# Performance work log

Measured on AMD Instinct MI355X. Metric: run time of the kernel, lower is better.

Reference implementation:

```python
import jax, jax.numpy as jnp
import numpy as np

V, E, U, D, B, T = 32000, 256, 512, 512, 32, 64


def setup_inputs() -> dict:
    key = jax.random.key(0)
    ks = jax.random.split(key, 12)
    g = lambda k, shape: (jax.random.normal(k, shape, jnp.float32) * 0.05)
    return dict(
        x=jax.random.randint(ks[0], (B, T), 0, V),
        emb=g(ks[1], (V, E)),
        Wxf=g(ks[2], (E, 4 * U)), Whf=g(ks[3], (U, 4 * U)), bf=jnp.zeros((4 * U,), jnp.float32),
        Wxb=g(ks[4], (E, 4 * U)), Whb=g(ks[5], (U, 4 * U)), bb=jnp.zeros((4 * U,), jnp.float32),
        W1=g(ks[6], (2 * U + D, 10)), b1=jnp.zeros((10,), jnp.float32),
        W2=g(ks[7], (10, 1)), b2=jnp.zeros((1,), jnp.float32),
        Wxd=g(ks[8], (2 * U, 4 * D)), Whd=g(ks[9], (D, 4 * D)), bd=jnp.zeros((4 * D,), jnp.float32),
        Wo=g(ks[10], (D, V)), bo=jnp.zeros((V,), jnp.float32),
    )


def lstm_cell(x_t, h, c, Wx, Wh, b):
    # Keras gate order: i, f, g(cell), o
    z = x_t @ Wx + h @ Wh + b
    i, f, g, o = jnp.split(z, 4, axis=-1)
    c = jax.nn.sigmoid(f) * c + jax.nn.sigmoid(i) * jnp.tanh(g)
    h = jax.nn.sigmoid(o) * jnp.tanh(c)
    return h, c


def lstm_seq(xs, Wx, Wh, b):
    # xs: [T, B, F] -> hidden states [T, B, units]
    units = Wh.shape[0]
    h0 = jnp.zeros((xs.shape[1], units), xs.dtype)

    def step(carry, x_t):
        h, c = lstm_cell(x_t, carry[0], carry[1], Wx, Wh, b)
        return (h, c), h

    _, hs = jax.lax.scan(step, (h0, h0), xs)
    return hs


def reference(x, emb, Wxf, Whf, bf, Wxb, Whb, bb, W1, b1, W2, b2, Wxd, Whd, bd, Wo, bo):
    Bsz, Tlen = x.shape
    xe = emb[x]                              # [B, T, E]
    xs = jnp.swapaxes(xe, 0, 1)              # [T, B, E]
    hf = lstm_seq(xs, Wxf, Whf, bf)          # forward direction
    hb = lstm_seq(xs[::-1], Wxb, Whb, bb)[::-1]  # backward direction
    a = jnp.swapaxes(jnp.concatenate([hf, hb], axis=-1), 0, 1)  # [B, T, 2U]
    du = Whd.shape[0]

    def dec_step(carry, _):
        h, c = carry
        s_rep = jnp.broadcast_to(h[:, None, :], (Bsz, Tlen, du))
        cat = jnp.concatenate([a, s_rep], axis=-1)              # [B, T, 2U+D]
        e = jax.nn.relu(jnp.tanh(cat @ W1 + b1) @ W2 + b2)      # [B, T, 1]
        score = jax.nn.softmax(e, axis=1)
        ctx = jnp.sum(score * a, axis=1)                        # [B, 2U]
        h, c = lstm_cell(ctx, h, c, Wxd, Whd, bd)
        out = jax.nn.softmax(h @ Wo + bo, axis=-1)              # [B, V]
        return (h, c), out

    init = (jnp.zeros((Bsz, du), a.dtype), jnp.zeros((Bsz, du), a.dtype))
    _, outs = jax.lax.scan(dec_step, init, None, length=Tlen)
    return jnp.swapaxes(outs, 0, 1)  # [B, T, V]
```

## Files before the change

### kernel.cpp

```cpp
#include <hip/hip_runtime.h>
#include <hip/hip_bf16.h>
#include <cstdint>

typedef float f32x4 __attribute__((ext_vector_type(4)));
typedef __bf16 bf16x8 __attribute__((ext_vector_type(8)));

__device__ __forceinline__ uint32_t bf1(float x) {
  uint32_t u = __float_as_uint(x);
  return (u + 0x7fffu + ((u >> 16) & 1u)) >> 16;
}
__device__ __forceinline__ uint32_t bpack(float lo, float hi) {
  return bf1(lo) | (bf1(hi) << 16);
}
__device__ __forceinline__ float blo(uint32_t u) { return __uint_as_float(u << 16); }
__device__ __forceinline__ float bhi(uint32_t u) { return __uint_as_float(u & 0xffff0000u); }
__device__ __forceinline__ float sigm(float x) {
  return __fdividef(1.f, 1.f + exp2f(x * -1.4426950408889634f));
}
__device__ __forceinline__ float tanhf_fast(float x) {
  float e2 = exp2f(x * 2.8853900817779268f);
  return 1.f - __fdividef(2.f, e2 + 1.f);
}

__device__ __forceinline__ float dot2bf(uint32_t a, uint32_t b, float acc) {
  asm("v_dot2_f32_bf16 %0, %1, %2, %0" : "+v"(acc) : "v"(a), "v"(b));
  return acc;
}

#define GLOAD_LDS16(g, l)                                                     \
  __builtin_amdgcn_global_load_lds(                                           \
      (const __attribute__((address_space(1))) void*)(g),                     \
      (__attribute__((address_space(3))) void*)(l), 16, 0, 0)

__global__ __launch_bounds__(256) void k0_pack(
    const float* __restrict__ Whf, const float* __restrict__ Whb,
    uint32_t* __restrict__ Wencp, const float* __restrict__ Whd,
    uint32_t* __restrict__ Wdp, const float* __restrict__ W1,
    uint32_t* __restrict__ W1pbAll)
{
  int bid = blockIdx.x;
  if (bid < 4096) {
    int p = bid * 256 + threadIdx.x;
    int j2 = p & 3, slot = (p >> 2) & 63, c = (p >> 8) & 15;
    int cg = (p >> 12) & 127, dir = p >> 19;
    int k = slot * 8 + j2 * 2;
    const float* W = dir ? Whb : Whf;
    int colg = (c >> 2) * 512 + cg * 4 + (c & 3);
    Wencp[p ^ ((c & 7) << 2)] =
        bpack(W[(size_t)k * 2048 + colg], W[(size_t)(k + 1) * 2048 + colg]);
  } else if (bid < 6144) {
    int p = (bid - 4096) * 256 + threadIdx.x;
    int e = p & 3, cc = (p >> 2) & 31, q4 = (p >> 7) & 63, ug = p >> 13;
    int k2 = 4 * q4 + e;
    int col = (cc >> 3) * 512 + ug * 8 + (cc & 7);
    int k = 2 * k2;
    Wdp[p] = bpack(Whd[(size_t)k * 2048 + col], Whd[(size_t)(k + 1) * 2048 + col]);
  } else {
    int p = (bid - 6144) * 256 + threadIdx.x;
    if (p < 9216) {
      int q = p / 12, j = p % 12;
      float v0 = (j < 10) ? W1[(size_t)(2 * q) * 10 + j] : 0.f;
      float v1 = (j < 10) ? W1[(size_t)(2 * q + 1) * 10 + j] : 0.f;
      W1pbAll[p] = bpack(v0, v1);
    }
  }
}

__global__ __launch_bounds__(256) void k1_embed_gemm(
    const int* __restrict__ x, const float* __restrict__ emb,
    const float* __restrict__ Wxf, const float* __restrict__ Wxb,
    const float* __restrict__ bfv, const float* __restrict__ bbv,
    float* __restrict__ Xf, float* __restrict__ Xb)
{
  __shared__ float As[32 * 260];
  __shared__ float Bs[32 * 128];
  __shared__ int xid[32];
  const int t = threadIdx.x;
  const int ty = blockIdx.y;
  const int c0 = blockIdx.x * 128;
  if (t < 32) xid[t] = x[t * 64 + ty];
  __syncthreads();
  for (int i = 0; i < 8; ++i) {
    int f4 = t + 256 * i;
    int r = f4 >> 6, k4 = (f4 & 63) << 2;
    float4 v = *(const float4*)(emb + (size_t)xid[r] * 256 + k4);
    *(float4*)(&As[r * 260 + k4]) = v;
  }
  const int isB = (c0 >= 2048);
  const float* Wsrc = isB ? Wxb : Wxf;
  const float* bias = isB ? bbv : bfv;
  const int cbase = c0 & 2047;
  float acc[4][4] = {};
  const int rq = t >> 5;
  const int cq = t & 31;
  for (int kc = 0; kc < 8; ++kc) {
    int k0 = kc * 32;
    __syncthreads();
    for (int i = 0; i < 4; ++i) {
      int f4 = t + 256 * i;
      int k = f4 >> 5, c4 = (f4 & 31) << 2;
      *(float4*)(&Bs[k * 128 + c4]) =
          *(const float4*)(Wsrc + (size_t)(k0 + k) * 2048 + cbase + c4);
    }
    __syncthreads();
#pragma unroll
    for (int kk = 0; kk < 32; ++kk) {
      float a0 = As[(4 * rq + 0) * 260 + k0 + kk];
      float a1 = As[(4 * rq + 1) * 260 + k0 + kk];
      float a2 = As[(4 * rq + 2) * 260 + k0 + kk];
      float a3 = As[(4 * rq + 3) * 260 + k0 + kk];
      float4 b = *(const float4*)(&Bs[kk * 128 + 4 * cq]);
      acc[0][0] += a0 * b.x; acc[0][1] += a0 * b.y; acc[0][2] += a0 * b.z; acc[0][3] += a0 * b.w;
      acc[1][0] += a1 * b.x; acc[1][1] += a1 * b.y; acc[1][2] += a1 * b.z; acc[1][3] += a1 * b.w;
      acc[2][0] += a2 * b.x; acc[2][1] += a2 * b.y; acc[2][2] += a2 * b.z; acc[2][3] += a2 * b.w;
      acc[3][0] += a3 * b.x; acc[3][1] += a3 * b.y; acc[3][2] += a3 * b.z; acc[3][3] += a3 * b.w;
    }
  }
  float* Xout = isB ? Xb : Xf;
  for (int i = 0; i < 4; ++i) {
    int c = cbase + 4 * cq + i;
    float bi = bias[c];
    for (int j = 0; j < 4; ++j) {
      int b_ = 4 * rq + j;
      Xout[((size_t)ty * 2048 + c) * 32 + b_] = acc[j][i] + bi;
    }
  }
}

__global__ __launch_bounds__(256) void k2_enc_step(
    const float* __restrict__ Xf, const float* __restrict__ Xb,
    const uint32_t* __restrict__ Wencp,
    const uint32_t* __restrict__ hfi, uint32_t* __restrict__ hfo,
    const uint32_t* __restrict__ hbi, uint32_t* __restrict__ hbo,
    float* __restrict__ cf, float* __restrict__ cb,
    ushort* __restrict__ aB, int step)
{
  __shared__ ushort Hs[16 * 512];
  __shared__ ushort Ws[16 * 512];
  __shared__ float zp[4 * 256];
  __shared__ float zx[256];
  __shared__ float zbuf[256];
  __shared__ float hl[64];
  const int t = threadIdx.x;
  const int dir = blockIdx.x >> 8;
  const int rh = (blockIdx.x >> 7) & 1;
  const int cg = blockIdx.x & 127;
  const int r0 = rh * 16, u0 = cg * 4;
  const float* XF = dir ? Xb : Xf;
  const uint32_t* hin = dir ? hbi : hfi;
  uint32_t* hout = dir ? hbo : hfo;
  float* cst = dir ? cb : cf;
  const int ta = dir ? (63 - step) : step;

  {
    const uint32_t* hinu = hin + r0 * 256;
    for (int i = 0; i < 4; ++i) {
      int b4 = (t >> 6) * 64 + 256 * i;
      GLOAD_LDS16(hinu + (size_t)(t + 256 * i) * 4, (uint32_t*)Hs + b4 * 4);
    }
    const uint32_t* wsrc = Wencp + ((size_t)dir * 128 + cg) * 4096;
    for (int i = 0; i < 4; ++i) {
      int b4 = (t >> 6) * 64 + 256 * i;
      GLOAD_LDS16(wsrc + (size_t)(t + 256 * i) * 4, (uint32_t*)Ws + b4 * 4);
    }
  }
  {
    int cl = t & 15, rl = t >> 4;
    int colg = (cl >> 2) * 512 + u0 + (cl & 3);
    zx[t] = XF[((size_t)ta * 2048 + colg) * 32 + r0 + rl];
  }
  __syncthreads();
  const int lane = t & 63, w = t >> 6;
  const int quad = lane >> 4, l15 = lane & 15;
  f32x4 acc = {};
#pragma unroll
  for (int mm = 0; mm < 4; ++mm) {
    int m = w * 4 + mm;
    int slot = m * 4 + quad;
    bf16x8 a = *(const bf16x8*)(Hs + l15 * 512 + (slot ^ (l15 & 7)) * 8);
    bf16x8 b = *(const bf16x8*)(Ws + l15 * 512 + (slot ^ (l15 & 7)) * 8);
    acc = __builtin_amdgcn_mfma_f32_16x16x32_bf16(a, b, acc, 0, 0, 0);
  }
#pragma unroll
  for (int reg = 0; reg < 4; ++reg)
    zp[w * 256 + (quad * 4 + reg) * 16 + l15] = acc[reg];
  __syncthreads();
  zbuf[t] = zp[t] + zp[256 + t] + zp[512 + t] + zp[768 + t] + zx[t];
  __syncthreads();
  if (t < 64) {
    int rl = t & 15, ui = t >> 4;
    int u = u0 + ui, r = r0 + rl;
    float zi = zbuf[rl * 16 + ui];
    float zf = zbuf[rl * 16 + 4 + ui];
    float zg = zbuf[rl * 16 + 8 + ui];
    float zo = zbuf[rl * 16 + 12 + ui];
    float cold = cst[u * 32 + r];
    float cn = sigm(zf) * cold + sigm(zi) * tanhf_fast(zg);
    float h = sigm(zo) * tanhf_fast(cn);
    cst[u * 32 + r] = cn;
    aB[((size_t)r * 64 + ta) * 1024 + dir * 512 + u] = (ushort)bf1(h);
    hl[rl * 4 + ui] = h;
  }
  __syncthreads();
  if (t < 16) {
    int r = r0 + t;
    uint32_t lo = bpack(hl[t * 4 + 0], hl[t * 4 + 1]);
    uint32_t hi = bpack(hl[t * 4 + 2], hl[t * 4 + 3]);
    uint32_t* dst = hout + r * 256 + (((cg >> 1) ^ (r & 7)) * 4) + (cg & 1) * 2;
    *(uint2*)dst = make_uint2(lo, hi);
  }
}

__global__ __launch_bounds__(256) void k5_aw1(
    const ushort* __restrict__ aB, const uint32_t* __restrict__ W1pbAll,
    const float* __restrict__ b1, float* __restrict__ aw1)
{
  __shared__ uint32_t ar[512];
  __shared__ float ps[16 * 17];
  const int t = threadIdx.x;
  const uint32_t* aBu = (const uint32_t*)aB;
  for (int m = blockIdx.x; m < 2048; m += gridDim.x) {
    __syncthreads();
    *(uint2*)(&ar[t * 2]) = *(const uint2*)(aBu + (size_t)m * 512 + t * 2);
    __syncthreads();
    int j = t & 15, part = t >> 4;
    int jj = j < 10 ? j : 0;
    float s = 0.f;
#pragma unroll 8
    for (int q = part * 32; q < part * 32 + 32; ++q)
      s = dot2bf(ar[q], W1pbAll[q * 12 + jj], s);
    ps[part * 17 + j] = s;
    __syncthreads();
    if (t < 16) {
      float sum = 0.f;
      if (t < 10) {
        for (int p = 0; p < 16; ++p) sum += ps[p * 17 + t];
        sum += b1[t];
      }
      aw1[m * 16 + t] = sum;
    }
  }
}

__global__ __launch_bounds__(256) void k_wxdT(
    const float* __restrict__ Wxd, ushort* __restrict__ WxdT)
{
  __shared__ float tile[64 * 65];
  const int t = threadIdx.x;
  const int n0 = blockIdx.x * 64, k0 = blockIdx.y * 64;
  for (int i = 0; i < 16; ++i) {
    int p = t + 256 * i;
    int kk = p >> 6, nn = p & 63;
    tile[kk * 65 + nn] = Wxd[(size_t)(k0 + kk) * 2048 + n0 + nn];
  }
  __syncthreads();
  for (int i = 0; i < 4; ++i) {
    int p = t + 256 * i;
    int nn = p >> 4, k4 = (p & 15) * 4;
    ushort4 o;
    o.x = (ushort)bf1(tile[(k4 + 0) * 65 + nn]);
    o.y = (ushort)bf1(tile[(k4 + 1) * 65 + nn]);
    o.z = (ushort)bf1(tile[(k4 + 2) * 65 + nn]);
    o.w = (ushort)bf1(tile[(k4 + 3) * 65 + nn]);
    *(ushort4*)(WxdT + (size_t)(n0 + nn) * 1024 + k0 + k4) = o;
  }
}

__global__ __launch_bounds__(256) void kA_aprime(
    const ushort* __restrict__ WxdT, const ushort* __restrict__ aB,
    uint32_t* __restrict__ ApTb)
{
  __shared__ ushort As[128 * 64];
  __shared__ ushort Bs[128 * 64];
  const int t = threadIdx.x;
  const int lane = t & 63, w = t >> 6;
  const int wr = w >> 1, wc = w & 1;
  const int m0 = blockIdx.y * 128, n0 = blockIdx.x * 128;
  const int lrow = lane >> 3, s = lane & 7;
  const int quad = lane >> 4, l15 = lane & 15;
  f32x4 acc[4][4] = {};
  for (int kc = 0; kc < 16; ++kc) {
    const int k0 = kc * 64;
    __syncthreads();
    for (int i = 0; i < 4; ++i) {
      int row = w * 32 + i * 8 + lrow;
      int k8 = s ^ (row & 7);
      GLOAD_LDS16(WxdT + (size_t)(m0 + row) * 1024 + k0 + k8 * 8,
                  As + (w * 32 + i * 8) * 64);
      GLOAD_LDS16(aB + (size_t)(n0 + row) * 1024 + k0 + k8 * 8,
                  Bs + (w * 32 + i * 8) * 64);
    }
    __syncthreads();
#pragma unroll
    for (int ks = 0; ks < 2; ++ks) {
      bf16x8 af[4], bfr[4];
      int kq = ks * 4 + quad;
#pragma unroll
      for (int mi = 0; mi < 4; ++mi) {
        int row = wr * 64 + mi * 16 + l15;
        int slot = kq ^ (row & 7);
        af[mi] = *(const bf16x8*)(As + row * 64 + slot * 8);
      }
#pragma unroll
      for (int ni = 0; ni < 4; ++ni) {
        int row = wc * 64 + ni * 16 + l15;
        int slot = kq ^ (row & 7);
        bfr[ni] = *(const bf16x8*)(Bs + row * 64 + slot * 8);
      }
#pragma unroll
      for (int mi = 0; mi < 4; ++mi)
#pragma unroll
        for (int ni = 0; ni < 4; ++ni)
          acc[mi][ni] = __builtin_amdgcn_mfma_f32_16x16x32_bf16(
              af[mi], bfr[ni], acc[mi][ni], 0, 0, 0);
    }
  }
#pragma unroll
  for (int mi = 0; mi < 4; ++mi) {
    int mbase = m0 + wr * 64 + mi * 16 + quad * 4;
#pragma unroll
    for (int reg = 0; reg < 4; ++reg) {
      int m = mbase + reg;
#pragma unroll
      for (int ni = 0; ni < 4; ++ni) {
        int n = n0 + wc * 64 + ni * 16 + l15;
        float v = acc[mi][ni][reg];
        float v2 = __shfl_xor(v, 1);
        if (!(l15 & 1))
          ApTb[(size_t)m * 1024 + (n >> 1)] = bpack(v, v2);
      }
    }
  }
}

__global__ __launch_bounds__(256) void k4_dec_step(
    const uint32_t* __restrict__ ApTb, const float* __restrict__ aw1,
    const uint32_t* __restrict__ W1pb, const float* __restrict__ W2,
    const float* __restrict__ b2, const uint32_t* __restrict__ hdp_in,
    const uint32_t* __restrict__ Wdp, const float* __restrict__ bd,
    uint32_t* __restrict__ hdp_out, float* __restrict__ cd,
    ushort* __restrict__ HsB, int step)
{
  __shared__ uint32_t W1s[256 * 12];
  __shared__ uint32_t hdT[1024];
  __shared__ uint32_t Wsp[8192];
  __shared__ float ph[64 * 4 * 12];
  __shared__ float hw1[4 * 12];
  __shared__ float esc[4 * 65];
  __shared__ uint32_t escp[4 * 33];
  __shared__ float pm[4 * 9];
  __shared__ float mrow[4], srow[4];
  __shared__ float w2s[12];
  __shared__ float zp[2][128];
  __shared__ float zbuf[4 * 33];
  __shared__ float hl[32];
  const int t = threadIdx.x;
  const int ug = blockIdx.x >> 3;
  const int rg = blockIdx.x & 7;
  const int u0 = ug * 8, r0 = rg * 4;
  for (int i = 0; i < 3; ++i) {
    int b4 = (t >> 6) * 64 + 256 * i;
    GLOAD_LDS16(W1pb + (size_t)(t + 256 * i) * 4, W1s + (size_t)b4 * 4);
  }
  {
    int q4 = t >> 2, rl0 = t & 3;
    int b4 = (t >> 6) * 64;
    GLOAD_LDS16(hdp_in + (size_t)(q4 * 32 + r0 + rl0) * 4, hdT + (size_t)b4 * 4);
  }
  if (t < 12) w2s[t] = (t < 10) ? W2[t] : 0.f;
  __syncthreads();
  {
    const uint32_t* wsrc = Wdp + (size_t)ug * 8192;
    for (int i = 0; i < 8; ++i) {
      int b4 = (t >> 6) * 64 + 256 * i;
      GLOAD_LDS16(wsrc + (size_t)(t + 256 * i) * 4, Wsp + (size_t)b4 * 4);
    }
  }
  {
    const int rl = t & 3, kp = t >> 2;
    const uint4* hd4 = (const uint4*)hdT;
    float acc[10] = {};
    {
      uint4 u4 = hd4[kp * 4 + rl];
      const uint32_t* w0 = &W1s[(4 * kp) * 12];
      const uint32_t* w1 = &W1s[(4 * kp + 1) * 12];
      const uint32_t* w2p = &W1s[(4 * kp + 2) * 12];
      const uint32_t* w3 = &W1s[(4 * kp + 3) * 12];
#pragma unroll
      for (int j = 0; j < 10; ++j) {
        acc[j] = dot2bf(u4.x, w0[j], acc[j]);
        acc[j] = dot2bf(u4.y, w1[j], acc[j]);
        acc[j] = dot2bf(u4.z, w2p[j], acc[j]);
        acc[j] = dot2bf(u4.w, w3[j], acc[j]);
      }
    }
#pragma unroll
    for (int j = 0; j < 10; ++j) ph[(kp * 4 + rl) * 12 + j] = acc[j];
  }
  __syncthreads();
  if (t < 40) {
    int rl = t / 10, j = t % 10;
    float s = 0.f;
#pragma unroll
    for (int p = 0; p < 64; ++p) s += ph[(p * 4 + rl) * 12 + j];
    hw1[rl * 12 + j] = s;
  }
  __syncthreads();
  const float b2v = b2[0];
  {
    int rl = t >> 6, tt = t & 63;
    size_t m = (size_t)(r0 + rl) * 64 + tt;
    const float4* aw = (const float4*)(aw1 + m * 16);
    float4 q0 = aw[0], q1 = aw[1], q2 = aw[2];
    const float* hw = &hw1[rl * 12];
    float e = b2v;
    e += tanhf_fast(q0.x + hw[0]) * w2s[0];
    e += tanhf_fast(q0.y + hw[1]) * w2s[1];
    e += tanhf_fast(q0.z + hw[2]) * w2s[2];
    e += tanhf_fast(q0.w + hw[3]) * w2s[3];
    e += tanhf_fast(q1.x + hw[4]) * w2s[4];
    e += tanhf_fast(q1.y + hw[5]) * w2s[5];
    e += tanhf_fast(q1.z + hw[6]) * w2s[6];
    e += tanhf_fast(q1.w + hw[7]) * w2s[7];
    e += tanhf_fast(q2.x + hw[8]) * w2s[8];
    e += tanhf_fast(q2.y + hw[9]) * w2s[9];
    esc[rl * 65 + tt] = fmaxf(e, 0.f);
  }
  __syncthreads();
  if (t < 32) {
    int rl = t >> 3, part = t & 7;
    float m = -1e30f;
    for (int i = 0; i < 8; ++i) m = fmaxf(m, esc[rl * 65 + part * 8 + i]);
    pm[rl * 9 + part] = m;
  }
  __syncthreads();
  if (t < 4) {
    float m = pm[t * 9];
    for (int p = 1; p < 8; ++p) m = fmaxf(m, pm[t * 9 + p]);
    mrow[t] = m;
  }
  __syncthreads();
  if (t < 32) {
    int rl = t >> 3, part = t & 7;
    float m = mrow[rl];
    float s = 0.f;
    for (int i = 0; i < 8; ++i) s += __expf(esc[rl * 65 + part * 8 + i] - m);
    pm[rl * 9 + part] = s;
  }
  __syncthreads();
  if (t < 4) {
    float s = 0.f;
    for (int p = 0; p < 8; ++p) s += pm[t * 9 + p];
    srow[t] = __fdividef(1.f, s);
  }
  __syncthreads();
  if (t < 128) {
    int rl = t >> 5, q = t & 31;
    float m = mrow[rl], s = srow[rl];
    float v0 = __expf(esc[rl * 65 + 2 * q] - m) * s;
    float v1 = __expf(esc[rl * 65 + 2 * q + 1] - m) * s;
    escp[rl * 33 + q] = bpack(v0, v1);
  }
  __syncthreads();
  {
    const int out = t & 127;
    const int ccB = out >> 2, rl = out & 3;
    const int kh = t >> 7;
    const int colg = (ccB >> 3) * 512 + u0 + (ccB & 7);
    float acc = 0.f;
    {
      const uint4* hd4 = (const uint4*)hdT;
      const uint4* wd4 = (const uint4*)Wsp;
#pragma unroll 8
      for (int q4 = kh * 32; q4 < kh * 32 + 32; ++q4) {
        uint4 ua = hd4[q4 * 4 + rl];
        uint4 ub = wd4[q4 * 32 + ccB];
        acc = dot2bf(ua.x, ub.x, acc);
        acc = dot2bf(ua.y, ub.y, acc);
        acc = dot2bf(ua.z, ub.z, acc);
        acc = dot2bf(ua.w, ub.w, acc);
      }
    }
    {
      const uint32_t* ap = ApTb + (size_t)colg * 1024 + (r0 + rl) * 32;
      const uint32_t* ep = &escp[rl * 33];
#pragma unroll
      for (int i8 = kh * 4; i8 < kh * 4 + 4; ++i8) {
        uint4 v = *(const uint4*)(ap + i8 * 4);
        acc = dot2bf(v.x, ep[4 * i8 + 0], acc);
        acc = dot2bf(v.y, ep[4 * i8 + 1], acc);
        acc = dot2bf(v.z, ep[4 * i8 + 2], acc);
        acc = dot2bf(v.w, ep[4 * i8 + 3], acc);
      }
    }
    zp[kh][out] = acc;
  }
  __syncthreads();
  if (t < 128) {
    int ccB = t >> 2, rl = t & 3;
    int colg = (ccB >> 3) * 512 + u0 + (ccB & 7);
    zbuf[rl * 33 + ccB] = zp[0][t] + zp[1][t] + bd[colg];
  }
  __syncthreads();
  if (t < 32) {
    int j = t >> 2, rr = t & 3;
    int u = u0 + j, rgl = r0 + rr;
    float zi = zbuf[rr * 33 + j];
    float zf = zbuf[rr * 33 + 8 + j];
    float zg = zbuf[rr * 33 + 16 + j];
    float zo = zbuf[rr * 33 + 24 + j];
    float cold = cd[u * 32 + rgl];
    float cn = sigm(zf) * cold + sigm(zi) * tanhf_fast(zg);
    float h = sigm(zo) * tanhf_fast(cn);
    cd[u * 32 + rgl] = cn;
    HsB[(size_t)(step * 32 + rgl) * 512 + u] = (ushort)bf1(h);
    hl[j * 4 + rr] = h;
  }
  __syncthreads();
  if (t < 16) {
    int p = t >> 2, rr = t & 3;
    hdp_out[ug * 128 + (r0 + rr) * 4 + p] =
        bpack(hl[(2 * p) * 4 + rr], hl[(2 * p + 1) * 4 + rr]);
  }
}

__global__ __launch_bounds__(256) void k_woT(
    const float* __restrict__ Wo, ushort* __restrict__ WoT)
{
  __shared__ float tile[64 * 65];
  const int t = threadIdx.x;
  const int n0 = blockIdx.x * 64, k0 = blockIdx.y * 64;
  for (int i = 0; i < 16; ++i) {
    int p = t + 256 * i;
    int kk = p >> 6, nn = p & 63;
    tile[kk * 65 + nn] = Wo[(size_t)(k0 + kk) * 32000 + n0 + nn];
  }
  __syncthreads();
  for (int i = 0; i < 4; ++i) {
    int p = t + 256 * i;
    int nn = p >> 4, k4 = (p & 15) * 4;
    ushort4 o;
    o.x = (ushort)bf1(tile[(k4 + 0) * 65 + nn]);
    o.y = (ushort)bf1(tile[(k4 + 1) * 65 + nn]);
    o.z = (ushort)bf1(tile[(k4 + 2) * 65 + nn]);
    o.w = (ushort)bf1(tile[(k4 + 3) * 65 + nn]);
    *(ushort4*)(WoT + (size_t)(n0 + nn) * 512 + k0 + k4) = o;
  }
}

__global__ __launch_bounds__(256) void k6_logits_mfma(
    const ushort* __restrict__ HsB, const ushort* __restrict__ WoT,
    const float* __restrict__ bo, float* __restrict__ out,
    float2* __restrict__ pstats, int moff)
{
  __shared__ ushort As[128 * 64];
  __shared__ ushort Bs[128 * 64];
  const int t = threadIdx.x;
  const int lane = t & 63, w = t >> 6;
  const int wr = w >> 1, wc = w & 1;
  const int m0 = (blockIdx.y + moff) * 128, n0 = blockIdx.x * 128;
  const int lrow = lane >> 3, s = lane & 7;
  const int quad = lane >> 4, l15 = lane & 15;
  f32x4 acc[4][4] = {};
  for (int kc = 0; kc < 8; ++kc) {
    const int k0 = kc * 64;
    __syncthreads();
    for (int i = 0; i < 4; ++i) {
      int row = w * 32 + i * 8 + lrow;
      int k8 = s ^ (row & 7);
      GLOAD_LDS16(HsB + (size_t)(m0 + row) * 512 + k0 + k8 * 8,
                  As + (w * 32 + i * 8) * 64);
      GLOAD_LDS16(WoT + (size_t)(n0 + row) * 512 + k0 + k8 * 8,
                  Bs + (w * 32 + i * 8) * 64);
    }
    __syncthreads();
#pragma unroll
    for (int ks = 0; ks < 2; ++ks) {
      bf16x8 af[4], bfr[4];
      int kq = ks * 4 + quad;
#pragma unroll
      for (int mi = 0; mi < 4; ++mi) {
        int row = wr * 64 + mi * 16 + l15;
        int slot = kq ^ (row & 7);
        af[mi] = *(const bf16x8*)(As + row * 64 + slot * 8);
      }
#pragma unroll
      for (int ni = 0; ni < 4; ++ni) {
        int row = wc * 64 + ni * 16 + l15;
        int slot = kq ^ (row & 7);
        bfr[ni] = *(const bf16x8*)(Bs + row * 64 + slot * 8);
      }
#pragma unroll
      for (int mi = 0; mi < 4; ++mi)
#pragma unroll
        for (int ni = 0; ni < 4; ++ni)
          acc[mi][ni] = __builtin_amdgcn_mfma_f32_16x16x32_bf16(
              af[mi], bfr[ni], acc[mi][ni], 0, 0, 0);
    }
  }
  __syncthreads();
  float* pmx = (float*)As;
  float* psm = (float*)Bs;
#pragma unroll
  for (int mi = 0; mi < 4; ++mi) {
    int mbase = m0 + wr * 64 + mi * 16 + quad * 4;
#pragma unroll
    for (int reg = 0; reg < 4; ++reg) {
      int m = mbase + reg;
      int rowl = (m - m0);
      size_t rowbase = ((size_t)(m & 31) * 64 + (m >> 5)) * 32000;
      float vs[4];
      float mx = -1e30f;
#pragma unroll
      for (int ni = 0; ni < 4; ++ni) {
        int n = n0 + wc * 64 + ni * 16 + l15;
        float v = acc[mi][ni][reg] + bo[n];
        out[rowbase + n] = v;
        vs[ni] = v;
        mx = fmaxf(mx, v);
      }
      float sl = __expf(vs[0] - mx) + __expf(vs[1] - mx) +
                 __expf(vs[2] - mx) + __expf(vs[3] - mx);
      pmx[rowl * 32 + wc * 16 + l15] = mx;
      psm[rowl * 32 + wc * 16 + l15] = sl;
    }
  }
  __syncthreads();
  if (t < 128) {
    float m = pmx[t * 32], sacc = psm[t * 32];
    for (int i = 1; i < 32; ++i) {
      float m2 = pmx[t * 32 + i], s2 = psm[t * 32 + i];
      float mn = fmaxf(m, m2);
      sacc = sacc * __expf(m - mn) + s2 * __expf(m2 - mn);
      m = mn;
    }
    int mg = m0 + t;
    int outrow = (mg & 31) * 64 + (mg >> 5);
    pstats[(size_t)outrow * 256 + blockIdx.x] = make_float2(m, sacc);
  }
}

__global__ __launch_bounds__(256) void k7_softmax(
    float* __restrict__ out, const float2* __restrict__ pstats, int half)
{
  __shared__ float mred[256], sred[256];
  const int t = threadIdx.x;
  const int mg = half * 1024 + blockIdx.x;
  const int row = (mg & 31) * 64 + (mg >> 5);
  float m = -1e30f, s = 0.f;
  if (t < 250) {
    float2 p = pstats[(size_t)row * 256 + t];
    m = p.x;
    s = p.y;
  }
  mred[t] = m;
  sred[t] = s;
  __syncthreads();
  for (int st = 128; st > 0; st >>= 1) {
    if (t < st) {
      float m1 = mred[t], m2 = mred[t + st];
      float mn = fmaxf(m1, m2);
      sred[t] = sred[t] * __expf(m1 - mn) + sred[t + st] * __expf(m2 - mn);
      mred[t] = mn;
    }
    __syncthreads();
  }
  m = mred[0];
  const float inv = 1.f / sred[0];
  float* p = out + (size_t)row * 32000;
  for (int i = t; i < 8000; i += 256) {
    float4 v = *(const float4*)(p + i * 4);
    v.x = __expf(v.x - m) * inv;
    v.y = __expf(v.y - m) * inv;
    v.z = __expf(v.z - m) * inv;
    v.w = __expf(v.w - m) * inv;
    *(float4*)(p + i * 4) = v;
  }
}

extern "C" void kernel_launch(void* const* d_in, const int* in_sizes, int n_in,
                              void* d_out, int out_size, void* d_ws, size_t ws_size,
                              hipStream_t stream)
{
  const int* x = (const int*)d_in[0];
  const float* emb = (const float*)d_in[1];
  const float* Wxf = (const float*)d_in[2];
  const float* Whf = (const float*)d_in[3];
  const float* bfv = (const float*)d_in[4];
  const float* Wxb = (const float*)d_in[5];
  const float* Whb = (const float*)d_in[6];
  const float* bbv = (const float*)d_in[7];
  const float* W1 = (const float*)d_in[8];
  const float* b1 = (const float*)d_in[9];
  const float* W2 = (const float*)d_in[10];
  const float* b2 = (const float*)d_in[11];
  const float* Wxd = (const float*)d_in[12];
  const float* Whd = (const float*)d_in[13];
  const float* bd = (const float*)d_in[14];
  const float* Wo = (const float*)d_in[15];
  const float* bo = (const float*)d_in[16];

  float* ws = (float*)d_ws;
  float* c_f = ws + 0;
  float* c_b = ws + 16384;
  float* c_d = ws + 32768;
  uint32_t* hfp0 = (uint32_t*)(ws + 49152);
  uint32_t* hfp1 = hfp0 + 8192;
  uint32_t* hbp0 = (uint32_t*)(ws + 65536);
  uint32_t* hbp1 = hbp0 + 8192;
  uint32_t* hdp0 = (uint32_t*)(ws + 81920);
  uint32_t* hdp1 = hdp0 + 8192;
  uint32_t* W1pbAll = (uint32_t*)(ws + 98304);
  uint32_t* Wencp = (uint32_t*)(ws + 114688);
  uint32_t* Wdp = (uint32_t*)(ws + 1163264);
  ushort* aB = (ushort*)(ws + 1687552);
  float* aw1 = ws + 2742272;
  float* Xf = ws + 2775040;
  float* Xb = Xf + 4194304;
  ushort* HsB = (ushort*)(ws + 13260800);
  uint32_t* ApTb = (uint32_t*)Xf;
  ushort* WxdT = (ushort*)Xb;
  ushort* WoT = (ushort*)Xf;
  float2* pstats = (float2*)Wencp;

  hipMemsetAsync(ws, 0, 98304 * sizeof(float), stream);

  k0_pack<<<6180, 256, 0, stream>>>(Whf, Whb, Wencp, Whd, Wdp, W1, W1pbAll);

  k1_embed_gemm<<<dim3(32, 64), 256, 0, stream>>>(x, emb, Wxf, Wxb, bfv, bbv, Xf, Xb);

  for (int s = 0; s < 64; ++s) {
    const uint32_t* hfi = (s & 1) ? hfp1 : hfp0;
    uint32_t* hfo = (s & 1) ? hfp0 : hfp1;
    const uint32_t* hbi = (s & 1) ? hbp1 : hbp0;
    uint32_t* hbo = (s & 1) ? hbp0 : hbp1;
    k2_enc_step<<<512, 256, 0, stream>>>(Xf, Xb, Wencp, hfi, hfo, hbi, hbo,
                                         c_f, c_b, aB, s);
  }

  k5_aw1<<<256, 256, 0, stream>>>(aB, W1pbAll, b1, aw1);
  k_wxdT<<<dim3(32, 16), 256, 0, stream>>>(Wxd, WxdT);
  kA_aprime<<<dim3(16, 16), 256, 0, stream>>>(WxdT, aB, ApTb);

  for (int s = 0; s < 64; ++s) {
    const uint32_t* hdi = (s & 1) ? hdp1 : hdp0;
    uint32_t* hdo = (s & 1) ? hdp0 : hdp1;
    k4_dec_step<<<512, 256, 0, stream>>>(ApTb, aw1, W1pbAll + 6144, W2, b2,
                                         hdi, Wdp, bd, hdo, c_d, HsB, s);
  }

  k_woT<<<dim3(500, 8), 256, 0, stream>>>(Wo, WoT);
  k6_logits_mfma<<<dim3(250, 8), 256, 0, stream>>>(HsB, WoT, bo,
                                                   (float*)d_out, pstats, 0);
  k7_softmax<<<1024, 256, 0, stream>>>((float*)d_out, pstats, 0);
  k6_logits_mfma<<<dim3(250, 8), 256, 0, stream>>>(HsB, WoT, bo,
                                                   (float*)d_out, pstats, 8);
  k7_softmax<<<1024, 256, 0, stream>>>((float*)d_out, pstats, 1);
}
```

Before: 1.527 ms.

## Move embedding input projection GEMM to bf16 MFMA and change Xf/Xb layout

Replaces the fp32 scalar-FMA embedding×Wx GEMM with a bf16 MFMA kernel that gathers embedding rows straight into LDS via async loads, converts them to bf16 on the fly, and uses pre-transposed bf16 weights made by a generic transpose kernel. The Xf/Xb output layout changes from [t][col][b] to [token][col], and the encoder step's read indexing is updated to match. The three separate transpose kernels are merged into one parameterised kernel. This removes a slow fp32 GEMM at the cost of two extra transpose launches and bf16 rounding of the input projection.

```diff
diff --git a/kernel.cpp b/kernel.cpp
--- a/kernel.cpp
+++ b/kernel.cpp
@@ -66,63 +66,115 @@
   }
 }
 
-__global__ __launch_bounds__(256) void k1_embed_gemm(
+__global__ __launch_bounds__(256) void k_wT(
+    const float* __restrict__ src, ushort* __restrict__ dst, int K, int N)
+{
+  __shared__ float tile[64 * 65];
+  const int t = threadIdx.x;
+  const int n0 = blockIdx.x * 64, k0 = blockIdx.y * 64;
+  for (int i = 0; i < 16; ++i) {
+    int p = t + 256 * i;
+    int kk = p >> 6, nn = p & 63;
+    tile[kk * 65 + nn] = src[(size_t)(k0 + kk) * N + n0 + nn];
+  }
+  __syncthreads();
+  for (int i = 0; i < 4; ++i) {
+    int p = t + 256 * i;
+    int nn = p >> 4, k4 = (p & 15) * 4;
+    ushort4 o;
+    o.x = (ushort)bf1(tile[(k4 + 0) * 65 + nn]);
+    o.y = (ushort)bf1(tile[(k4 + 1) * 65 + nn]);
+    o.z = (ushort)bf1(tile[(k4 + 2) * 65 + nn]);
+    o.w = (ushort)bf1(tile[(k4 + 3) * 65 + nn]);
+    *(ushort4*)(dst + (size_t)(n0 + nn) * K + k0 + k4) = o;
+  }
+}
+
+__global__ __launch_bounds__(256) void k1_embed_mfma(
     const int* __restrict__ x, const float* __restrict__ emb,
-    const float* __restrict__ Wxf, const float* __restrict__ Wxb,
+    const ushort* __restrict__ WxfT, const ushort* __restrict__ WxbT,
     const float* __restrict__ bfv, const float* __restrict__ bbv,
     float* __restrict__ Xf, float* __restrict__ Xb)
 {
-  __shared__ float As[32 * 260];
-  __shared__ float Bs[32 * 128];
-  __shared__ int xid[32];
+  __shared__ float Afp[128 * 64];
+  __shared__ ushort Bs[128 * 64];
+  __shared__ int xid[128];
   const int t = threadIdx.x;
-  const int ty = blockIdx.y;
-  const int c0 = blockIdx.x * 128;
-  if (t < 32) xid[t] = x[t * 64 + ty];
-  __syncthreads();
-  for (int i = 0; i < 8; ++i) {
-    int f4 = t + 256 * i;
-    int r = f4 >> 6, k4 = (f4 & 63) << 2;
-    float4 v = *(const float4*)(emb + (size_t)xid[r] * 256 + k4);
-    *(float4*)(&As[r * 260 + k4]) = v;
-  }
-  const int isB = (c0 >= 2048);
-  const float* Wsrc = isB ? Wxb : Wxf;
+  const int n0g = blockIdx.x * 128;
+  const int m0 = blockIdx.y * 128;
+  const int isB = (n0g >= 2048);
+  const int n0 = n0g & 2047;
+  const ushort* WT = isB ? WxbT : WxfT;
   const float* bias = isB ? bbv : bfv;
-  const int cbase = c0 & 2047;
-  float acc[4][4] = {};
-  const int rq = t >> 5;
-  const int cq = t & 31;
-  for (int kc = 0; kc < 8; ++kc) {
-    int k0 = kc * 32;
-    __syncthreads();
+  if (t < 128) xid[t] = x[m0 + t];
+  __syncthreads();
+  int xr[8];
+#pragma unroll
+  for (int i = 0; i < 8; ++i) xr[i] = xid[(t >> 4) + 16 * i];
+  const int lane = t & 63, w = t >> 6;
+  const int quad = lane >> 4, l15 = lane & 15;
+  f32x4 acc[2][8] = {};
+  for (int kc = 0; kc < 4; ++kc) {
+    const int k0 = kc * 64;
+    __syncthreads();
+    for (int i = 0; i < 8; ++i) {
+      int idx = t + 256 * i;
+      int row = (t >> 4) + 16 * i, ch = idx & 15;
+      int gr = (ch >> 1) ^ (row & 7), w16 = ch & 1;
+      GLOAD_LDS16(emb + (size_t)xr[i] * 256 + k0 + gr * 8 + w16 * 4,
+                  Afp + idx * 4);
+    }
     for (int i = 0; i < 4; ++i) {
-      int f4 = t + 256 * i;
-      int k = f4 >> 5, c4 = (f4 & 31) << 2;
-      *(float4*)(&Bs[k * 128 + c4]) =
-          *(const float4*)(Wsrc + (size_t)(k0 + k) * 2048 + cbase + c4);
-    }
-    __syncthreads();
-#pragma unroll
-    for (int kk = 0; kk < 32; ++kk) {
-      float a0 = As[(4 * rq + 0) * 260 + k0 + kk];
-      float a1 = As[(4 * rq + 1) * 260 + k0 + kk];
-      float a2 = As[(4 * rq + 2) * 260 + k0 + kk];
-      float a3 = As[(4 * rq + 3) * 260 + k0 + kk];
-      float4 b = *(const float4*)(&Bs[kk * 128 + 4 * cq]);
-      acc[0][0] += a0 * b.x; acc[0][1] += a0 * b.y; acc[0][2] += a0 * b.z; acc[0][3] += a0 * b.w;
-      acc[1][0] += a1 * b.x; acc[1][1] += a1 * b.y; acc[1][2] += a1 * b.z; acc[1][3] += a1 * b.w;
-      acc[2][0] += a2 * b.x; acc[2][1] += a2 * b.y; acc[2][2] += a2 * b.z; acc[2][3] += a2 * b.w;
-      acc[3][0] += a3 * b.x; acc[3][1] += a3 * b.y; acc[3][2] += a3 * b.z; acc[3][3] += a3 * b.w;
+      int idx = t + 256 * i;
+      int row = idx >> 3, s8 = (idx & 7) ^ (row & 7);
+      GLOAD_LDS16(WT + (size_t)(n0 + row) * 256 + k0 + s8 * 8,
+                  Bs + idx * 8);
+    }
+    __syncthreads();
+#pragma unroll
+    for (int ks = 0; ks < 2; ++ks) {
+      int kq = ks * 4 + quad;
+      bf16x8 af[2];
+#pragma unroll
+      for (int mi = 0; mi < 2; ++mi) {
+        int row = w * 32 + mi * 16 + l15;
+        int slot = kq ^ (row & 7);
+        const float* ap = Afp + row * 64 + slot * 8;
+        float4 a0 = *(const float4*)ap;
+        float4 a1 = *(const float4*)(ap + 4);
+        union { ushort u[8]; bf16x8 v; } cv;
+        cv.u[0] = (ushort)bf1(a0.x); cv.u[1] = (ushort)bf1(a0.y);
+        cv.u[2] = (ushort)bf1(a0.z); cv.u[3] = (ushort)bf1(a0.w);
+        cv.u[4] = (ushort)bf1(a1.x); cv.u[5] = (ushort)bf1(a1.y);
+        cv.u[6] = (ushort)bf1(a1.z); cv.u[7] = (ushort)bf1(a1.w);
+        af[mi] = cv.v;
+      }
+#pragma unroll
+      for (int ni = 0; ni < 8; ++ni) {
+        int rowB = ni * 16 + l15;
+        int slotB = kq ^ (rowB & 7);
+        bf16x8 bfr = *(const bf16x8*)(Bs + rowB * 64 + slotB * 8);
+#pragma unroll
+        for (int mi = 0; mi < 2; ++mi)
+          acc[mi][ni] = __builtin_amdgcn_mfma_f32_16x16x32_bf16(
+              af[mi], bfr, acc[mi][ni], 0, 0, 0);
+      }
     }
   }
   float* Xout = isB ? Xb : Xf;
-  for (int i = 0; i < 4; ++i) {
-    int c = cbase + 4 * cq + i;
-    float bi = bias[c];
-    for (int j = 0; j < 4; ++j) {
-      int b_ = 4 * rq + j;
-      Xout[((size_t)ty * 2048 + c) * 32 + b_] = acc[j][i] + bi;
+  float bcol[8];
+#pragma unroll
+  for (int ni = 0; ni < 8; ++ni) bcol[ni] = bias[n0 + ni * 16 + l15];
+#pragma unroll
+  for (int mi = 0; mi < 2; ++mi) {
+#pragma unroll
+    for (int reg = 0; reg < 4; ++reg) {
+      int token = m0 + w * 32 + mi * 16 + quad * 4 + reg;
+#pragma unroll
+      for (int ni = 0; ni < 8; ++ni) {
+        int col = n0 + ni * 16 + l15;
+        Xout[(size_t)token * 2048 + col] = acc[mi][ni][reg] + bcol[ni];
+      }
     }
   }
 }
@@ -167,7 +219,7 @@
   {
     int cl = t & 15, rl = t >> 4;
     int colg = (cl >> 2) * 512 + u0 + (cl & 3);
-    zx[t] = XF[((size_t)ta * 2048 + colg) * 32 + r0 + rl];
+    zx[t] = XF[(size_t)((r0 + rl) * 64 + ta) * 2048 + colg];
   }
   __syncthreads();
   const int lane = t & 63, w = t >> 6;
@@ -239,30 +291,6 @@
       }
       aw1[m * 16 + t] = sum;
     }
-  }
-}
-
-__global__ __launch_bounds__(256) void k_wxdT(
-    const float* __restrict__ Wxd, ushort* __restrict__ WxdT)
-{
-  __shared__ float tile[64 * 65];
-  const int t = threadIdx.x;
-  const int n0 = blockIdx.x * 64, k0 = blockIdx.y * 64;
-  for (int i = 0; i < 16; ++i) {
-    int p = t + 256 * i;
-    int kk = p >> 6, nn = p & 63;
-    tile[kk * 65 + nn] = Wxd[(size_t)(k0 + kk) * 2048 + n0 + nn];
-  }
-  __syncthreads();
-  for (int i = 0; i < 4; ++i) {
-    int p = t + 256 * i;
-    int nn = p >> 4, k4 = (p & 15) * 4;
-    ushort4 o;
-    o.x = (ushort)bf1(tile[(k4 + 0) * 65 + nn]);
-    o.y = (ushort)bf1(tile[(k4 + 1) * 65 + nn]);
-    o.z = (ushort)bf1(tile[(k4 + 2) * 65 + nn]);
-    o.w = (ushort)bf1(tile[(k4 + 3) * 65 + nn]);
-    *(ushort4*)(WxdT + (size_t)(n0 + nn) * 1024 + k0 + k4) = o;
   }
 }
 
@@ -524,30 +552,6 @@
   }
 }
 
-__global__ __launch_bounds__(256) void k_woT(
-    const float* __restrict__ Wo, ushort* __restrict__ WoT)
-{
-  __shared__ float tile[64 * 65];
-  const int t = threadIdx.x;
-  const int n0 = blockIdx.x * 64, k0 = blockIdx.y * 64;
-  for (int i = 0; i < 16; ++i) {
-    int p = t + 256 * i;
-    int kk = p >> 6, nn = p & 63;
-    tile[kk * 65 + nn] = Wo[(size_t)(k0 + kk) * 32000 + n0 + nn];
-  }
-  __syncthreads();
-  for (int i = 0; i < 4; ++i) {
-    int p = t + 256 * i;
-    int nn = p >> 4, k4 = (p & 15) * 4;
-    ushort4 o;
-    o.x = (ushort)bf1(tile[(k4 + 0) * 65 + nn]);
-    o.y = (ushort)bf1(tile[(k4 + 1) * 65 + nn]);
-    o.z = (ushort)bf1(tile[(k4 + 2) * 65 + nn]);
-    o.w = (ushort)bf1(tile[(k4 + 3) * 65 + nn]);
-    *(ushort4*)(WoT + (size_t)(n0 + nn) * 512 + k0 + k4) = o;
-  }
-}
-
 __global__ __launch_bounds__(256) void k6_logits_mfma(
     const ushort* __restrict__ HsB, const ushort* __restrict__ WoT,
     const float* __restrict__ bo, float* __restrict__ out,
@@ -717,6 +721,8 @@
   float* aw1 = ws + 2742272;
   float* Xf = ws + 2775040;
   float* Xb = Xf + 4194304;
+  ushort* WxfT = (ushort*)(ws + 11163648);
+  ushort* WxbT = (ushort*)(ws + 11425792);
   ushort* HsB = (ushort*)(ws + 13260800);
   uint32_t* ApTb = (uint32_t*)Xf;
   ushort* WxdT = (ushort*)Xb;
@@ -726,8 +732,11 @@
   hipMemsetAsync(ws, 0, 98304 * sizeof(float), stream);
 
   k0_pack<<<6180, 256, 0, stream>>>(Whf, Whb, Wencp, Whd, Wdp, W1, W1pbAll);
-
-  k1_embed_gemm<<<dim3(32, 64), 256, 0, stream>>>(x, emb, Wxf, Wxb, bfv, bbv, Xf, Xb);
+  k_wT<<<dim3(32, 4), 256, 0, stream>>>(Wxf, WxfT, 256, 2048);
+  k_wT<<<dim3(32, 4), 256, 0, stream>>>(Wxb, WxbT, 256, 2048);
+
+  k1_embed_mfma<<<dim3(32, 16), 256, 0, stream>>>(x, emb, WxfT, WxbT,
+                                                  bfv, bbv, Xf, Xb);
 
   for (int s = 0; s < 64; ++s) {
     const uint32_t* hfi = (s & 1) ? hfp1 : hfp0;
@@ -739,7 +748,7 @@
   }
 
   k5_aw1<<<256, 256, 0, stream>>>(aB, W1pbAll, b1, aw1);
-  k_wxdT<<<dim3(32, 16), 256, 0, stream>>>(Wxd, WxdT);
+  k_wT<<<dim3(32, 16), 256, 0, stream>>>(Wxd, WxdT, 1024, 2048);
   kA_aprime<<<dim3(16, 16), 256, 0, stream>>>(WxdT, aB, ApTb);
 
   for (int s = 0; s < 64; ++s) {
@@ -749,7 +758,7 @@
                                          hdi, Wdp, bd, hdo, c_d, HsB, s);
   }
 
-  k_woT<<<dim3(500, 8), 256, 0, stream>>>(Wo, WoT);
+  k_wT<<<dim3(500, 8), 256, 0, stream>>>(Wo, WoT, 512, 32000);
   k6_logits_mfma<<<dim3(250, 8), 256, 0, stream>>>(HsB, WoT, bo,
                                                    (float*)d_out, pstats, 0);
   k7_softmax<<<1024, 256, 0, stream>>>((float*)d_out, pstats, 0);
```

New measurement: 1.479 ms. -3.2%, faster.
